# Kernel tuning notes

Hardware: AMD Instinct MI355X
Metric: run time of the kernel (lower is better)

## Reference

```python
import jax, jax.numpy as jnp
import numpy as np

B, S, D, H = 8, 1024, 1024, 16
DK = D // H  # 64


def setup_inputs() -> dict:
    key = jax.random.key(0)
    k1, k2, k3, k4, k5, k6 = jax.random.split(key, 6)
    mask = jax.random.randint(k1, (B, S, S), 0, 2, dtype=jnp.int32)
    x_key_value = jax.random.normal(k2, (B, S, D), dtype=jnp.float32)
    # per-head projection weights (stacked over heads)
    scale = 1.0 / np.sqrt(D)
    wq = jax.random.normal(k3, (H, D, DK), dtype=jnp.float32) * scale
    wk = jax.random.normal(k4, (H, D, DK), dtype=jnp.float32) * scale
    wv = jax.random.normal(k5, (H, D, DK), dtype=jnp.float32) * scale
    # output projection (nn.Parameter; randomized here for a meaningful baseline)
    wo = jax.random.normal(k6, (D, D), dtype=jnp.float32) * scale
    return {"mask": mask, "x_key_value": x_key_value, "wq": wq, "wk": wk, "wv": wv, "wo": wo}


def reference(mask, x_key_value, wq, wk, wv, wo):
    # batched multi-head SDPA (equivalent to the per-head Python loop + concat)
    q = jnp.einsum('bsd,hdk->bhsk', x_key_value, wq)
    k = jnp.einsum('btd,hdk->bhtk', x_key_value, wk)
    v = jnp.einsum('btd,hdk->bhtk', x_key_value, wv)
    scores = jnp.einsum('bhsk,bhtk->bhst', q, k) / jnp.sqrt(jnp.asarray(DK, q.dtype))
    scores = jnp.where(mask[:, None, :, :] != 0, scores, jnp.asarray(-1e9, q.dtype))
    attn = jax.nn.softmax(scores, axis=-1)
    ctx = jnp.einsum('bhst,bhtk->bhsk', attn, v)
    # concat heads along feature dim: [B,S,H*DK]
    ctx = ctx.transpose(0, 2, 1, 3).reshape(B, S, D)
    # output proj (dropout is identity in eval) + residual
    res = ctx @ wo + x_key_value
    # torch.layer_norm over normalized_shape = (S, D), no affine, eps=1e-5
    mean = jnp.mean(res, axis=(1, 2), keepdims=True)
    var = jnp.var(res, axis=(1, 2), keepdims=True)
    return (res - mean) / jnp.sqrt(var + 1e-5)
```

## Files before the change

### kernel.cpp

```cpp
#include <hip/hip_runtime.h>

typedef unsigned short u16;
typedef __attribute__((ext_vector_type(8))) short bf16x8;
typedef __attribute__((ext_vector_type(4))) float f32x4;


static __device__ __forceinline__ u16 f2bf(float f) {
    union { float f; unsigned u; } v; v.f = f;
    unsigned r = v.u + 0x7fffu + ((v.u >> 16) & 1u);
    return (u16)(r >> 16);
}

static __device__ __forceinline__ f32x4 mfma16(bf16x8 a, bf16x8 b, f32x4 c) {
    return __builtin_amdgcn_mfma_f32_16x16x32_bf16(a, b, c, 0, 0, 0);
}

static __device__ __forceinline__ void load_lds16(const u16* g, u16* l) {
    __builtin_amdgcn_global_load_lds((const __attribute__((address_space(1))) unsigned*)(const void*)g,
                                     (__attribute__((address_space(3))) unsigned*)(void*)l, 16, 0, 0);
}

__global__ __launch_bounds__(256) void prep_kernel(const float* __restrict__ x,
                                                   const float* __restrict__ wq, const float* __restrict__ wk,
                                                   const float* __restrict__ wv, const float* __restrict__ wo,
                                                   const int* __restrict__ mask,
                                                   u16* __restrict__ xb, u16* __restrict__ wt,
                                                   u16* __restrict__ wot, uint2* __restrict__ mb,
                                                   float* __restrict__ sums) {
    int bid = blockIdx.x;
    if (bid == 0 && threadIdx.x < 16) sums[threadIdx.x] = 0.f;
    if (bid < 8192) {
        int i = (bid * 256 + threadIdx.x) * 4;
        float4 v = *(const float4*)(x + i);
        ushort4 o;
        o.x = f2bf(v.x); o.y = f2bf(v.y); o.z = f2bf(v.z); o.w = f2bf(v.w);
        *(ushort4*)(xb + i) = o;
    } else if (bid < 24576) {
        int o = (bid - 8192) * 256 + threadIdx.x;
        if (o < 3145728) {
            int z = o >> 20;
            int rem = o & 1048575;
            int n = rem >> 10;
            int d = rem & 1023;
            int h = n >> 6, kk = n & 63;
            const float* w = (z == 0) ? wq : (z == 1) ? wk : wv;
            wt[o] = f2bf(w[h * 65536 + d * 64 + kk]);
        } else {
            int oo = o - 3145728;
            int n = oo >> 10, d = oo & 1023;
            wot[oo] = f2bf(wo[d * 1024 + n]);
        }
    } else {
        long long wi = (long long)(bid - 24576) * 4 + (threadIdx.x >> 6);
        int lane = threadIdx.x & 63;
        int v = mask[wi * 64 + lane];
        unsigned long long bal = __ballot(v != 0);
        if (lane == 0) {
            uint2 o; o.x = (unsigned)bal; o.y = (unsigned)(bal >> 32);
            mb[wi] = o;
        }
    }
}

__global__ __launch_bounds__(256) void qkv_gemm_kernel(const u16* __restrict__ xb, const u16* __restrict__ wt,
                                                       u16* __restrict__ qb, u16* __restrict__ kb,
                                                       u16* __restrict__ vtb) {
    __shared__ __align__(16) u16 As[128 * 64];
    __shared__ __align__(16) u16 Bs[128 * 64];

    int t = threadIdx.x;
    int lane = t & 63, w = t >> 6;
    int wm = w & 1, wn = w >> 1;
    int l16 = lane & 15, quad = lane >> 4;
    int sw = l16 & 7;

    int m0 = blockIdx.x * 128;
    int n0g = blockIdx.y * 128;

    int srow = t >> 3;
    int skp = ((t & 7) ^ (srow & 7)) * 8;
    const u16* ga0 = xb + (m0 + srow) * 1024 + skp;
    const u16* gb0 = wt + (n0g + srow) * 1024 + skp;

    int arow0 = wm * 64 + l16;
    int brow0 = wn * 64 + l16;

    f32x4 acc[4][4];
#pragma unroll
    for (int i = 0; i < 4; ++i)
#pragma unroll
        for (int j = 0; j < 4; ++j) acc[i][j] = (f32x4){0.f, 0.f, 0.f, 0.f};

    for (int kb0 = 0; kb0 < 1024; kb0 += 64) {
        __syncthreads();
#pragma unroll
        for (int c = 0; c < 4; ++c)
            load_lds16(ga0 + c * 32768 + kb0, &As[c * 2048 + t * 8]);
#pragma unroll
        for (int c = 0; c < 4; ++c)
            load_lds16(gb0 + c * 32768 + kb0, &Bs[c * 2048 + t * 8]);
        __syncthreads();

#pragma unroll
        for (int kh = 0; kh < 2; ++kh) {
            int kidx = ((kh << 2) + quad) ^ sw;
            bf16x8 af[4], bfr[4];
#pragma unroll
            for (int i = 0; i < 4; ++i)
                af[i] = *(const bf16x8*)&As[(arow0 + i * 16) * 64 + kidx * 8];
#pragma unroll
            for (int j = 0; j < 4; ++j)
                bfr[j] = *(const bf16x8*)&Bs[(brow0 + j * 16) * 64 + kidx * 8];
#pragma unroll
            for (int i = 0; i < 4; ++i)
#pragma unroll
                for (int j = 0; j < 4; ++j)
                    acc[i][j] = mfma16(af[i], bfr[j], acc[i][j]);
        }
    }

    int z = blockIdx.y >> 3;
    float qscale = (z == 0) ? 0.125f : 1.0f;
#pragma unroll
    for (int j = 0; j < 4; ++j) {
        int ng = n0g + wn * 64 + j * 16 + l16;
        int nl = ng & 1023;
        int h = nl >> 6, kk = nl & 63;
#pragma unroll
        for (int i = 0; i < 4; ++i) {
#pragma unroll
            for (int r = 0; r < 4; ++r) {
                int m = m0 + wm * 64 + i * 16 + quad * 4 + r;
                int b_ = m >> 10, s = m & 1023;
                u16 val = f2bf(acc[i][j][r] * qscale);
                if (z == 0)      qb[((b_ * 16 + h) * 1024 + s) * 64 + kk] = val;
                else if (z == 1) kb[((b_ * 16 + h) * 1024 + s) * 64 + kk] = val;
                else             vtb[((b_ * 16 + h) * 64 + kk) * 1024 + s] = val;
            }
        }
    }
}

__global__ __launch_bounds__(256) void attn_kernel(const u16* __restrict__ qb, const u16* __restrict__ kb,
                                                   const u16* __restrict__ vtb, const uint2* __restrict__ mb,
                                                   u16* __restrict__ ctx) {
    __shared__ __align__(16) u16 Ks[64 * 64];
    __shared__ __align__(16) u16 Vs[64 * 64];
    __shared__ __align__(16) u16 P[4][16][72];

    int t = threadIdx.x;
    int w = t >> 6, lane = t & 63;
    int l16 = lane & 15, quad = lane >> 4;
    int h = blockIdx.y, b = blockIdx.z;
    int q0 = blockIdx.x * 64 + w * 16;

    const u16* Q = qb + (b * 16 + h) * 65536;
    const u16* K = kb + (b * 16 + h) * 65536;
    const u16* Vt = vtb + (b * 16 + h) * 65536;
    const uint2* MB = mb + (b * 1024 + q0) * 16;

    int srow = t >> 3;
    int skp = ((t & 7) ^ (srow & 7)) * 8;
    const u16* gk0 = K + srow * 64 + skp;
    const u16* gv0 = Vt + srow * 1024 + skp;

    bf16x8 qf0 = *(const bf16x8*)(Q + (q0 + l16) * 64 + quad * 8);
    bf16x8 qf1 = *(const bf16x8*)(Q + (q0 + l16) * 64 + 32 + quad * 8);

    f32x4 O[4];
#pragma unroll
    for (int j = 0; j < 4; ++j) O[j] = (f32x4){0.f, 0.f, 0.f, 0.f};
    float lsum[4] = {0.f, 0.f, 0.f, 0.f};

    int sw = l16 & 7;

    for (int kt0 = 0; kt0 < 16; ++kt0) {
        int k0 = kt0 * 64;

        uint2 mw[4];
#pragma unroll
        for (int r = 0; r < 4; ++r)
            mw[r] = MB[(quad * 4 + r) * 16 + kt0];

        __syncthreads();
#pragma unroll
        for (int c = 0; c < 2; ++c) {
            load_lds16(gk0 + (k0 + c * 32) * 64, &Ks[c * 2048 + t * 8]);
            load_lds16(gv0 + c * 32 * 1024 + k0, &Vs[c * 2048 + t * 8]);
        }
        __syncthreads();

        f32x4 s[4];
#pragma unroll
        for (int kt = 0; kt < 4; ++kt) {
            int row = kt * 16 + l16;
            bf16x8 klo = *(const bf16x8*)&Ks[row * 64 + ((quad ^ sw) * 8)];
            bf16x8 khi = *(const bf16x8*)&Ks[row * 64 + (((4 + quad) ^ sw) * 8)];
            f32x4 z = {0.f, 0.f, 0.f, 0.f};
            z = mfma16(qf0, klo, z);
            z = mfma16(qf1, khi, z);
            s[kt] = z;
        }

#pragma unroll
        for (int r = 0; r < 4; ++r) {
            int qrow = quad * 4 + r;
#pragma unroll
            for (int kt = 0; kt < 4; ++kt) {
                unsigned wsel = (kt < 2) ? mw[r].x : mw[r].y;
                unsigned bit = (wsel >> ((kt & 1) * 16 + l16)) & 1u;
                float e = bit ? __expf(s[kt][r]) : 0.f;
                lsum[r] += e;
                P[w][qrow][kt * 16 + l16] = f2bf(e);
            }
        }

        bf16x8 pf0 = *(const bf16x8*)&P[w][l16][quad * 8];
        bf16x8 pf1 = *(const bf16x8*)&P[w][l16][32 + quad * 8];

#pragma unroll
        for (int j = 0; j < 4; ++j) {
            int row = j * 16 + l16;
            bf16x8 vlo = *(const bf16x8*)&Vs[row * 64 + ((quad ^ sw) * 8)];
            bf16x8 vhi = *(const bf16x8*)&Vs[row * 64 + (((4 + quad) ^ sw) * 8)];
            O[j] = mfma16(pf0, vlo, O[j]);
            O[j] = mfma16(pf1, vhi, O[j]);
        }
    }

#pragma unroll
    for (int r = 0; r < 4; ++r) {
        float s = lsum[r];
        s += __shfl_xor(s, 1);
        s += __shfl_xor(s, 2);
        s += __shfl_xor(s, 4);
        s += __shfl_xor(s, 8);
        lsum[r] = s;
    }

#pragma unroll
    for (int r = 0; r < 4; ++r) {
        int sI = q0 + quad * 4 + r;
        float inv = 1.0f / lsum[r];
        int base = (b * 1024 + sI) * 1024 + h * 64;
#pragma unroll
        for (int j = 0; j < 4; ++j)
            ctx[base + j * 16 + l16] = f2bf(O[j][r] * inv);
    }
}

__global__ __launch_bounds__(256) void oproj_gemm_kernel(const u16* __restrict__ ctxb, const u16* __restrict__ wot,
                                                         const float* __restrict__ x, float* __restrict__ res,
                                                         float* __restrict__ sums) {
    __shared__ __align__(16) u16 As[128 * 64];
    __shared__ __align__(16) u16 Bs[128 * 64];

    int t = threadIdx.x;
    int lane = t & 63, w = t >> 6;
    int wm = w & 1, wn = w >> 1;
    int l16 = lane & 15, quad = lane >> 4;
    int sw = l16 & 7;

    int m0 = blockIdx.x * 128;
    int n0 = blockIdx.y * 128;

    int srow = t >> 3;
    int skp = ((t & 7) ^ (srow & 7)) * 8;
    const u16* ga0 = ctxb + (m0 + srow) * 1024 + skp;
    const u16* gb0 = wot + (n0 + srow) * 1024 + skp;

    int arow0 = wm * 64 + l16;
    int brow0 = wn * 64 + l16;

    f32x4 acc[4][4];
#pragma unroll
    for (int i = 0; i < 4; ++i)
#pragma unroll
        for (int j = 0; j < 4; ++j) acc[i][j] = (f32x4){0.f, 0.f, 0.f, 0.f};

    for (int kb0 = 0; kb0 < 1024; kb0 += 64) {
        __syncthreads();
#pragma unroll
        for (int c = 0; c < 4; ++c)
            load_lds16(ga0 + c * 32768 + kb0, &As[c * 2048 + t * 8]);
#pragma unroll
        for (int c = 0; c < 4; ++c)
            load_lds16(gb0 + c * 32768 + kb0, &Bs[c * 2048 + t * 8]);
        __syncthreads();

#pragma unroll
        for (int kh = 0; kh < 2; ++kh) {
            int kidx = ((kh << 2) + quad) ^ sw;
            bf16x8 af[4], bfr[4];
#pragma unroll
            for (int i = 0; i < 4; ++i)
                af[i] = *(const bf16x8*)&As[(arow0 + i * 16) * 64 + kidx * 8];
#pragma unroll
            for (int j = 0; j < 4; ++j)
                bfr[j] = *(const bf16x8*)&Bs[(brow0 + j * 16) * 64 + kidx * 8];
#pragma unroll
            for (int i = 0; i < 4; ++i)
#pragma unroll
                for (int j = 0; j < 4; ++j)
                    acc[i][j] = mfma16(af[i], bfr[j], acc[i][j]);
        }
    }

    float ps = 0.f, ps2 = 0.f;
#pragma unroll
    for (int i = 0; i < 4; ++i) {
#pragma unroll
        for (int r = 0; r < 4; ++r) {
            int m = m0 + wm * 64 + i * 16 + quad * 4 + r;
#pragma unroll
            for (int j = 0; j < 4; ++j) {
                int n = n0 + wn * 64 + j * 16 + l16;
                float v = acc[i][j][r] + x[m * 1024 + n];
                res[m * 1024 + n] = v;
                ps += v; ps2 += v * v;
            }
        }
    }

#pragma unroll
    for (int off = 32; off > 0; off >>= 1) {
        ps += __shfl_xor(ps, off);
        ps2 += __shfl_xor(ps2, off);
    }
    __shared__ float ls[4], ls2[4];
    if (lane == 0) { ls[w] = ps; ls2[w] = ps2; }
    __syncthreads();
    if (t == 0) {
        int b = blockIdx.x >> 3;
        atomicAdd(&sums[b * 2 + 0], ls[0] + ls[1] + ls[2] + ls[3]);
        atomicAdd(&sums[b * 2 + 1], ls2[0] + ls2[1] + ls2[2] + ls2[3]);
    }
}

__global__ __launch_bounds__(256) void norm_kernel(const float* __restrict__ res, const float* __restrict__ sums,
                                                   float* __restrict__ out) {
    int i = (blockIdx.x * 256 + threadIdx.x) * 4;
    int b = i >> 20;
    float mean = sums[b * 2 + 0] * (1.0f / 1048576.0f);
    float var = sums[b * 2 + 1] * (1.0f / 1048576.0f) - mean * mean;
    float rs = rsqrtf(var + 1e-5f);
    float4 v = *(const float4*)(res + i);
    float4 o;
    o.x = (v.x - mean) * rs;
    o.y = (v.y - mean) * rs;
    o.z = (v.z - mean) * rs;
    o.w = (v.w - mean) * rs;
    *(float4*)(out + i) = o;
}


extern "C" void kernel_launch(void* const* d_in, const int* in_sizes, int n_in,
                              void* d_out, int out_size, void* d_ws, size_t ws_size,
                              hipStream_t stream) {
    const int* mask  = (const int*)d_in[0];
    const float* x   = (const float*)d_in[1];
    const float* wq  = (const float*)d_in[2];
    const float* wk  = (const float*)d_in[3];
    const float* wv  = (const float*)d_in[4];
    const float* wo  = (const float*)d_in[5];
    float* out = (float*)d_out;

    char* ws = (char*)d_ws;
    u16* xb    = (u16*)(ws + 0);
    u16* wt    = (u16*)(ws + 16777216);
    u16* wot   = (u16*)(ws + 23068672);
    u16* qb    = (u16*)(ws + 25165824);
    u16* kb    = (u16*)(ws + 41943040);
    u16* vtb   = (u16*)(ws + 58720256);
    float* res = (float*)(ws + 25165824);
    float* sums = (float*)(ws + 75497472);
    uint2* mbits = (uint2*)(ws + 76546048);
    u16* ctxb  = (u16*)d_out;

    prep_kernel<<<57344, 256, 0, stream>>>(x, wq, wk, wv, wo, mask, xb, wt, wot, mbits, sums);
    qkv_gemm_kernel<<<dim3(64, 24), 256, 0, stream>>>(xb, wt, qb, kb, vtb);
    attn_kernel<<<dim3(16, 16, 8), 256, 0, stream>>>(qb, kb, vtb, mbits, ctxb);
    oproj_gemm_kernel<<<dim3(64, 8), 256, 0, stream>>>(ctxb, wot, x, res, sums);
    norm_kernel<<<8192, 256, 0, stream>>>(res, sums, out);
}
```

Baseline: 336.4 us.

## Use exp2 with folded log2e, MFMA row sums, and smaller o-proj tiles

Folds log2(e) into the Q scale so the attention softmax can use exp2 directly. P is converted to bf16 by truncation instead of rounding, and the row sum is computed with an extra MFMA against a ones vector, so the sum matches the bf16 P values and the shuffle reduction is gone. Separately, the output-projection GEMM switches to 64x128 tiles with twice as many blocks, which improves CU occupancy on a grid that was only 512 blocks. The risks are slightly different rounding from truncation and two more MFMAs per tile in the attention loop.

After: 346.1 us. +2.9%, slower.

```diff
diff --git a/kernel.cpp b/kernel.cpp
--- a/kernel.cpp
+++ b/kernel.cpp
@@ -120,7 +120,7 @@
     }
 
     int z = blockIdx.y >> 3;
-    float qscale = (z == 0) ? 0.125f : 1.0f;
+    float qscale = (z == 0) ? 0.125f * 1.44269504088896f : 1.0f;
 #pragma unroll
     for (int j = 0; j < 4; ++j) {
         int ng = n0g + wn * 64 + j * 16 + l16;
@@ -167,10 +167,14 @@
     bf16x8 qf0 = *(const bf16x8*)(Q + (q0 + l16) * 64 + quad * 8);
     bf16x8 qf1 = *(const bf16x8*)(Q + (q0 + l16) * 64 + 32 + quad * 8);
 
+    bf16x8 ones;
+#pragma unroll
+    for (int i = 0; i < 8; ++i) ones[i] = (short)0x3F80;
+
     f32x4 O[4];
 #pragma unroll
     for (int j = 0; j < 4; ++j) O[j] = (f32x4){0.f, 0.f, 0.f, 0.f};
-    float lsum[4] = {0.f, 0.f, 0.f, 0.f};
+    f32x4 Osum = {0.f, 0.f, 0.f, 0.f};
 
     int sw = l16 & 7;
 
@@ -209,9 +213,10 @@
             for (int kt = 0; kt < 4; ++kt) {
                 unsigned wsel = (kt < 2) ? mw[r].x : mw[r].y;
                 unsigned bit = (wsel >> ((kt & 1) * 16 + l16)) & 1u;
-                float e = bit ? __expf(s[kt][r]) : 0.f;
-                lsum[r] += e;
-                P[w][qrow][kt * 16 + l16] = f2bf(e);
+                float ex = __builtin_exp2f(s[kt][r]);
+                union { float f; unsigned u; } cv;
+                cv.f = bit ? ex : 0.f;
+                P[w][qrow][kt * 16 + l16] = (u16)(cv.u >> 16);
             }
         }
 
@@ -226,22 +231,14 @@
             O[j] = mfma16(pf0, vlo, O[j]);
             O[j] = mfma16(pf1, vhi, O[j]);
         }
-    }
-
-#pragma unroll
-    for (int r = 0; r < 4; ++r) {
-        float s = lsum[r];
-        s += __shfl_xor(s, 1);
-        s += __shfl_xor(s, 2);
-        s += __shfl_xor(s, 4);
-        s += __shfl_xor(s, 8);
-        lsum[r] = s;
+        Osum = mfma16(pf0, ones, Osum);
+        Osum = mfma16(pf1, ones, Osum);
     }
 
 #pragma unroll
     for (int r = 0; r < 4; ++r) {
         int sI = q0 + quad * 4 + r;
-        float inv = 1.0f / lsum[r];
+        float inv = 1.0f / Osum[r];
         int base = (b * 1024 + sI) * 1024 + h * 64;
 #pragma unroll
         for (int j = 0; j < 4; ++j)
@@ -252,16 +249,15 @@
 __global__ __launch_bounds__(256) void oproj_gemm_kernel(const u16* __restrict__ ctxb, const u16* __restrict__ wot,
                                                          const float* __restrict__ x, float* __restrict__ res,
                                                          float* __restrict__ sums) {
-    __shared__ __align__(16) u16 As[128 * 64];
+    __shared__ __align__(16) u16 As[64 * 64];
     __shared__ __align__(16) u16 Bs[128 * 64];
 
     int t = threadIdx.x;
     int lane = t & 63, w = t >> 6;
-    int wm = w & 1, wn = w >> 1;
     int l16 = lane & 15, quad = lane >> 4;
     int sw = l16 & 7;
 
-    int m0 = blockIdx.x * 128;
+    int m0 = blockIdx.x * 64;
     int n0 = blockIdx.y * 128;
 
     int srow = t >> 3;
@@ -269,19 +265,16 @@
     const u16* ga0 = ctxb + (m0 + srow) * 1024 + skp;
     const u16* gb0 = wot + (n0 + srow) * 1024 + skp;
 
-    int arow0 = wm * 64 + l16;
-    int brow0 = wn * 64 + l16;
-
-    f32x4 acc[4][4];
+    f32x4 acc[4][2];
 #pragma unroll
     for (int i = 0; i < 4; ++i)
 #pragma unroll
-        for (int j = 0; j < 4; ++j) acc[i][j] = (f32x4){0.f, 0.f, 0.f, 0.f};
+        for (int j = 0; j < 2; ++j) acc[i][j] = (f32x4){0.f, 0.f, 0.f, 0.f};
 
     for (int kb0 = 0; kb0 < 1024; kb0 += 64) {
         __syncthreads();
 #pragma unroll
-        for (int c = 0; c < 4; ++c)
+        for (int c = 0; c < 2; ++c)
             load_lds16(ga0 + c * 32768 + kb0, &As[c * 2048 + t * 8]);
 #pragma unroll
         for (int c = 0; c < 4; ++c)
@@ -291,17 +284,17 @@
 #pragma unroll
         for (int kh = 0; kh < 2; ++kh) {
             int kidx = ((kh << 2) + quad) ^ sw;
-            bf16x8 af[4], bfr[4];
+            bf16x8 af[4], bfr[2];
 #pragma unroll
             for (int i = 0; i < 4; ++i)
-                af[i] = *(const bf16x8*)&As[(arow0 + i * 16) * 64 + kidx * 8];
-#pragma unroll
-            for (int j = 0; j < 4; ++j)
-                bfr[j] = *(const bf16x8*)&Bs[(brow0 + j * 16) * 64 + kidx * 8];
+                af[i] = *(const bf16x8*)&As[(i * 16 + l16) * 64 + kidx * 8];
+#pragma unroll
+            for (int j = 0; j < 2; ++j)
+                bfr[j] = *(const bf16x8*)&Bs[(w * 32 + j * 16 + l16) * 64 + kidx * 8];
 #pragma unroll
             for (int i = 0; i < 4; ++i)
 #pragma unroll
-                for (int j = 0; j < 4; ++j)
+                for (int j = 0; j < 2; ++j)
                     acc[i][j] = mfma16(af[i], bfr[j], acc[i][j]);
         }
     }
@@ -311,10 +304,10 @@
     for (int i = 0; i < 4; ++i) {
 #pragma unroll
         for (int r = 0; r < 4; ++r) {
-            int m = m0 + wm * 64 + i * 16 + quad * 4 + r;
-#pragma unroll
-            for (int j = 0; j < 4; ++j) {
-                int n = n0 + wn * 64 + j * 16 + l16;
+            int m = m0 + i * 16 + quad * 4 + r;
+#pragma unroll
+            for (int j = 0; j < 2; ++j) {
+                int n = n0 + w * 32 + j * 16 + l16;
                 float v = acc[i][j][r] + x[m * 1024 + n];
                 res[m * 1024 + n] = v;
                 ps += v; ps2 += v * v;
@@ -331,7 +324,7 @@
     if (lane == 0) { ls[w] = ps; ls2[w] = ps2; }
     __syncthreads();
     if (t == 0) {
-        int b = blockIdx.x >> 3;
+        int b = blockIdx.x >> 4;
         atomicAdd(&sums[b * 2 + 0], ls[0] + ls[1] + ls[2] + ls[3]);
         atomicAdd(&sums[b * 2 + 1], ls2[0] + ls2[1] + ls2[2] + ls2[3]);
     }
@@ -380,6 +373,6 @@
     prep_kernel<<<57344, 256, 0, stream>>>(x, wq, wk, wv, wo, mask, xb, wt, wot, mbits, sums);
     qkv_gemm_kernel<<<dim3(64, 24), 256, 0, stream>>>(xb, wt, qb, kb, vtb);
     attn_kernel<<<dim3(16, 16, 8), 256, 0, stream>>>(qb, kb, vtb, mbits, ctxb);
-    oproj_gemm_kernel<<<dim3(64, 8), 256, 0, stream>>>(ctxb, wot, x, res, sums);
+    oproj_gemm_kernel<<<dim3(128, 8), 256, 0, stream>>>(ctxb, wot, x, res, sums);
     norm_kernel<<<8192, 256, 0, stream>>>(res, sums, out);
 }
```
